# Performance work log

Measured on AMD Instinct MI355X. Metric: run time of the kernel, lower is better.

Reference implementation:

```python
import jax, jax.numpy as jnp
from jax import lax
import numpy as np

T, N, C, S = 256, 64, 7356, 32
NEG = -1e9  # finite stand-in for -inf (keeps grads clean)


def setup_inputs() -> dict:
    key = jax.random.key(0)
    k1, k2, k3 = jax.random.split(key, 3)
    out = jax.random.normal(k1, (T, N, C), dtype=jnp.float32)
    # PyTorch CTCLoss expects log-probs; the module passes `out` through as-is,
    # so we feed log_softmax'd activations (what the surrounding model produces).
    out = jax.nn.log_softmax(out, axis=-1)
    text = jax.random.randint(k2, (N, S), 1, C)            # labels in [1, C-1], blank=0 excluded
    pre_len = jnp.full((N,), T, dtype=jnp.int64 if jax.config.jax_enable_x64 else jnp.int32)
    lengths = jax.random.randint(k3, (N,), 16, S + 1)       # target lengths in [16, 32]
    return {"out": out, "text": text, "pre_len": pre_len, "lengths": lengths}


def _ctc_loss_mean(logp, targets, input_lengths, target_lengths):
    # logp: [T, N, C] log-probs; targets: [N, S]; lengths: [N]
    Tt, Nn, _ = logp.shape
    Ss = targets.shape[1]
    L = 2 * Ss + 1
    # Extended label sequence: blank, l1, blank, l2, ..., blank
    ext = jnp.zeros((Nn, L), dtype=targets.dtype).at[:, 1::2].set(targets)  # [N, L]
    ext_m2 = jnp.concatenate([jnp.zeros((Nn, 2), dtype=ext.dtype), ext[:, :-2]], axis=1)
    skip = (jnp.arange(L)[None, :] >= 2) & (ext != 0) & (ext != ext_m2)      # [N, L]

    # Gather per-frame log-probs of extended labels: [T, N, L]
    lp_ext = logp[:, jnp.arange(Nn)[:, None], ext]

    alpha0 = jnp.full((Nn, L), NEG, dtype=logp.dtype)
    alpha0 = alpha0.at[:, 0].set(lp_ext[0, :, 0]).at[:, 1].set(lp_ext[0, :, 1])

    negcol1 = jnp.full((Nn, 1), NEG, dtype=logp.dtype)
    negcol2 = jnp.full((Nn, 2), NEG, dtype=logp.dtype)

    def step(alpha, lp_t):
        s1 = jnp.concatenate([negcol1, alpha[:, :-1]], axis=1)
        s2 = jnp.concatenate([negcol2, alpha[:, :-2]], axis=1)
        a = jnp.logaddexp(alpha, s1)
        a = jnp.logaddexp(a, jnp.where(skip, s2, NEG))
        new = a + lp_t
        return new, new

    _, alphas_rest = lax.scan(step, alpha0, lp_ext[1:])
    alphas = jnp.concatenate([alpha0[None], alphas_rest], axis=0)  # [T, N, L]

    n_idx = jnp.arange(Nn)
    a_end = alphas[input_lengths - 1, n_idx]                        # [N, L]
    l_last = 2 * target_lengths                                     # index of final blank
    log_like = jnp.logaddexp(a_end[n_idx, l_last], a_end[n_idx, l_last - 1])
    # reduction='mean': per-sample loss / target_length, then mean over batch
    per = -log_like / target_lengths.astype(logp.dtype)
    return jnp.mean(per)


def reference(out, text, pre_len, lengths):
    loss = _ctc_loss_mean(out, text, pre_len, lengths)
    weight = jnp.square(1.0 - jnp.exp(-loss))
    return weight * loss
```

## Files before the change

### kernel.cpp

```cpp
#include <hip/hip_runtime.h>

#define Tt 256
#define Nn 64
#define Cc 7356
#define Ss 32
#define NEGf (-1.0e9f)
#define LOG2E 1.4426950408889634f
#define LN2   0.6931471805599453f
#define PFD 16
#define HT 128

__device__ __forceinline__ float fexp2(float x) { return __builtin_amdgcn_exp2f(x); }
__device__ __forceinline__ float flog2(float x) { return __builtin_amdgcn_logf(x); }

__device__ __forceinline__ float dpp_shr1(float x, float fallback) {
    int r = __builtin_amdgcn_update_dpp(__float_as_int(fallback), __float_as_int(x),
                                        0x138 , 0xf, 0xf, false);
    return __int_as_float(r);
}
__device__ __forceinline__ float dpp_shl1(float x, float fallback) {
    int r = __builtin_amdgcn_update_dpp(__float_as_int(fallback), __float_as_int(x),
                                        0x130 , 0xf, 0xf, false);
    return __int_as_float(r);
}
__device__ __forceinline__ float bcast(float x, int l) {
    return __int_as_float(__builtin_amdgcn_readlane(__float_as_int(x), l));
}
__device__ __forceinline__ float lse2(float a, float b) {
    float m = fmaxf(a, b);
    return m + flog2(fexp2(a - m) + fexp2(b - m));
}

#define COMPACT_FLOATS (Tt * Nn * 64)
#define JV_OFF COMPACT_FLOATS
#define WS_NEED_BYTES ((COMPACT_FLOATS + Nn + 1) * 4)

__global__ __launch_bounds__(256) void ctc_gather_kernel(
    const float* __restrict__ logp, const int* __restrict__ text,
    float* __restrict__ ws)
{
    int gid = blockIdx.x * 256 + threadIdx.x;
    int l  = gid & 63;
    int n  = (gid >> 6) & (Nn - 1);
    int tq = gid >> 12;
    int ch = (l & 1) ? 0 : text[n * Ss + (l >> 1)];
    const float* src = logp + (size_t)n * Cc + ch;
    const size_t tstr = (size_t)Nn * Cc;
    float v0 = src[(size_t)(4 * tq + 0) * tstr];
    float v1 = src[(size_t)(4 * tq + 1) * tstr];
    float v2 = src[(size_t)(4 * tq + 2) * tstr];
    float v3 = src[(size_t)(4 * tq + 3) * tstr];
    float* dst = ws + (size_t)n * 64 + l;
    dst[(size_t)(4 * tq + 0) * (Nn * 64)] = v0 * LOG2E;
    dst[(size_t)(4 * tq + 1) * (Nn * 64)] = v1 * LOG2E;
    dst[(size_t)(4 * tq + 2) * (Nn * 64)] = v2 * LOG2E;
    dst[(size_t)(4 * tq + 3) * (Nn * 64)] = v3 * LOG2E;
    if (gid == 0) {
        int* counter = (int*)(ws + JV_OFF + Nn);
        __hip_atomic_store(counter, 0, __ATOMIC_RELAXED, __HIP_MEMORY_SCOPE_AGENT);
    }
}

__global__ __launch_bounds__(128) void ctc_fbj_kernel(
    const float* __restrict__ compact, const int* __restrict__ text,
    const int* __restrict__ lengths, float* __restrict__ ws,
    float* __restrict__ out)
{
    __shared__ float jpre[65];
    __shared__ float jbeta[65];

    const int lane = threadIdx.x & 63;
    const bool fwd = threadIdx.x < 64;
    const int n    = blockIdx.x;

    int ch = (lane & 1) ? 0 : text[n * Ss + (lane >> 1)];
    int ch_m2 = __shfl_up(ch, 2, 64);
    int ch_p2 = __shfl_down(ch, 2, 64);
    const bool skipd = (lane >= 2) && !(lane & 1) && (ch != ch_m2);
    const bool skips = !(lane & 1) && (lane <= 61) && (ch != ch_p2);

    const float* base = compact + (size_t)n * 64 + lane;
    const int rstride = Nn * 64;
    const int len = lengths[n];

    float stv;
    float st0;

    if (fwd) {
        float lp0 = base[0];
        stv = (lane == 0) ? lp0 : NEGf;
        st0 = bcast(lp0, 1);
        float lpb[PFD];
        #pragma unroll
        for (int i = 0; i < PFD; ++i)
            lpb[i] = base[(size_t)(1 + i) * rstride];
        int t = 1;
        for (int blk = 0; blk < 7; ++blk) {
            #pragma unroll
            for (int j = 0; j < PFD; ++j) {
                float lp = lpb[j];
                int tpf = t + PFD;
                if (tpf <= HT - 1)
                    lpb[j] = base[(size_t)tpf * rstride];
                float lpblank = bcast(lp, 1);
                float s1 = dpp_shr1(stv, st0);
                float s2 = dpp_shr1(s1, NEGf);
                float s2m = skipd ? s2 : NEGf;
                float m  = fmaxf(fmaxf(stv, s1), s2m);
                float e  = fexp2(stv - m) + fexp2(s1 - m) + fexp2(s2m - m);
                stv = (m + lp) + flog2(e);
                st0 = st0 + lpblank;
                ++t;
            }
        }
        #pragma unroll
        for (int j = 0; j < PFD - 1; ++j) {
            float lp = lpb[j];
            float lpblank = bcast(lp, 1);
            float s1 = dpp_shr1(stv, st0);
            float s2 = dpp_shr1(s1, NEGf);
            float s2m = skipd ? s2 : NEGf;
            float m  = fmaxf(fmaxf(stv, s1), s2m);
            float e  = fexp2(stv - m) + fexp2(s1 - m) + fexp2(s2m - m);
            stv = (m + lp) + flog2(e);
            st0 = st0 + lpblank;
        }
        float s1 = dpp_shr1(stv, st0);
        float s2 = dpp_shr1(s1, NEGf);
        float s2m = skipd ? s2 : NEGf;
        float m  = fmaxf(fmaxf(stv, s1), s2m);
        float e  = fexp2(stv - m) + fexp2(s1 - m) + fexp2(s2m - m);
        jpre[1 + lane] = m + flog2(e);
        if (lane == 0) jpre[0] = st0;
    } else {
        float lpT = base[(size_t)(Tt - 1) * rstride];
        int llast = 2 * len;
        stv = (lane == llast - 2 || lane == llast - 1) ? lpT : NEGf;
        st0 = NEGf;
        float lpb[PFD];
        #pragma unroll
        for (int i = 0; i < PFD; ++i)
            lpb[i] = base[(size_t)(Tt - 2 - i) * rstride];
        int t = Tt - 2;
        for (int blk = 0; blk < 7; ++blk) {
            #pragma unroll
            for (int j = 0; j < PFD; ++j) {
                float lp = lpb[j];
                int tpf = t - PFD;
                if (tpf >= HT)
                    lpb[j] = base[(size_t)tpf * rstride];
                float lpblank = bcast(lp, 1);
                float b1 = bcast(stv, 0);
                float u1 = dpp_shl1(stv, NEGf);
                float u2 = dpp_shl1(u1, NEGf);
                float u2m = skips ? u2 : NEGf;
                float m  = fmaxf(fmaxf(stv, u1), u2m);
                float e  = fexp2(stv - m) + fexp2(u1 - m) + fexp2(u2m - m);
                float nb = (m + lp) + flog2(e);
                float m2 = fmaxf(st0, b1);
                st0 = (m2 + lpblank) + flog2(fexp2(st0 - m2) + fexp2(b1 - m2));
                stv = nb;
                --t;
            }
        }
        #pragma unroll
        for (int j = 0; j < PFD - 1; ++j) {
            float lp = lpb[j];
            float lpblank = bcast(lp, 1);
            float b1 = bcast(stv, 0);
            float u1 = dpp_shl1(stv, NEGf);
            float u2 = dpp_shl1(u1, NEGf);
            float u2m = skips ? u2 : NEGf;
            float m  = fmaxf(fmaxf(stv, u1), u2m);
            float e  = fexp2(stv - m) + fexp2(u1 - m) + fexp2(u2m - m);
            float nb = (m + lp) + flog2(e);
            float m2 = fmaxf(st0, b1);
            st0 = (m2 + lpblank) + flog2(fexp2(st0 - m2) + fexp2(b1 - m2));
            stv = nb;
        }
        jbeta[1 + lane] = stv;
        if (lane == 0) jbeta[0] = st0;
    }

    __syncthreads();
    if (!fwd) return;

    float local = jpre[lane] + jbeta[lane];
    if (lane == 0) local = lse2(local, jpre[64] + jbeta[64]);
    #pragma unroll
    for (int off = 1; off < 64; off <<= 1)
        local = lse2(local, __shfl_xor(local, off, 64));
    float per = -(local * LN2) / (float)len;

    float* slots = ws + JV_OFF;
    int* counter = (int*)(ws + JV_OFF + Nn);
    int old = -1;
    if (lane == 0) {
        __hip_atomic_store(&slots[n], per, __ATOMIC_RELEASE, __HIP_MEMORY_SCOPE_AGENT);
        __threadfence();
        old = __hip_atomic_fetch_add(counter, 1, __ATOMIC_ACQ_REL, __HIP_MEMORY_SCOPE_AGENT);
    }
    old = __shfl(old, 0, 64);
    if (old == Nn - 1) {
        __threadfence();
        float v = __hip_atomic_load(&slots[lane], __ATOMIC_ACQUIRE, __HIP_MEMORY_SCOPE_AGENT);
        #pragma unroll
        for (int off = 32; off > 0; off >>= 1)
            v += __shfl_down(v, off, 64);
        if (lane == 0) {
            float loss = v * (1.0f / (float)Nn);
            float w = 1.0f - __expf(-loss);
            out[0] = w * w * loss;
        }
    }
}

__global__ __launch_bounds__(64) void ctc_alpha_kernel(
    const float* __restrict__ logp, const int* __restrict__ text,
    const int* __restrict__ pre_len, const int* __restrict__ lengths,
    float* __restrict__ per_out)
{
    const int n = blockIdx.x; const int lane = threadIdx.x;
    int ch = 0;
    if (lane & 1) ch = text[n * Ss + (lane >> 1)];
    int ch_m2 = __shfl_up(ch, 2, 64);
    bool skip = (lane >= 2) && (ch != 0) && (ch != ch_m2);
    const size_t rowbase = (size_t)n * Cc, tstride = (size_t)Nn * Cc;
    float lp0 = logp[rowbase + ch] * LOG2E;
    float alpha = (lane < 2) ? lp0 : NEGf, alpha64 = NEGf;
    const int stop_t = pre_len[n] - 1;
    float sv = alpha, sv64 = alpha64;
    float lpb[PFD];
    #pragma unroll
    for (int i = 0; i < PFD; ++i)
        lpb[i] = logp[(size_t)(1 + i) * tstride + rowbase + ch] * LOG2E;
#define CTC_STEP(LPREG) { \
        float lp = (LPREG); float lpblank = bcast(lp, 0); float a63 = bcast(alpha, 63); \
        float s1 = dpp_shr1(alpha, NEGf); float s2 = dpp_shr1(s1, NEGf); \
        float s2m = skip ? s2 : NEGf; \
        float m = fmaxf(fmaxf(alpha, s1), s2m); \
        float e = fexp2(alpha - m) + fexp2(s1 - m) + fexp2(s2m - m); \
        float na = (m + lp) + flog2(e); \
        float m2 = fmaxf(alpha64, a63); \
        alpha64 = (m2 + lpblank) + flog2(fexp2(alpha64 - m2) + fexp2(a63 - m2)); \
        alpha = na; if (t == stop_t) { sv = alpha; sv64 = alpha64; } ++t; }
    int t = 1;
    for (int blk = 0; blk < 15; ++blk) {
        #pragma unroll
        for (int j = 0; j < PFD; ++j) {
            float lpj = lpb[j]; int tpf = t + PFD;
            if (tpf < Tt) lpb[j] = logp[(size_t)tpf * tstride + rowbase + ch] * LOG2E;
            CTC_STEP(lpj);
        }
    }
    #pragma unroll
    for (int j = 0; j < PFD - 1; ++j) { CTC_STEP(lpb[j]); }
#undef CTC_STEP
    int len = lengths[n]; int l_last = 2 * len;
    float v1 = __shfl(sv, l_last < 64 ? l_last : 63, 64);
    if (l_last == 64) v1 = sv64;
    float v2 = __shfl(sv, l_last - 1, 64);
    float per = -(lse2(v1, v2) * LN2) / (float)len;
    if (lane == 0) per_out[n] = per;
}

__global__ __launch_bounds__(64) void finalize_kernel(
    const float* __restrict__ per, float* __restrict__ out)
{
    int lane = threadIdx.x;
    float v = per[lane];
    #pragma unroll
    for (int off = 32; off > 0; off >>= 1) v += __shfl_down(v, off, 64);
    if (lane == 0) {
        float loss = v * (1.0f / (float)Nn);
        float w = 1.0f - __expf(-loss);
        out[0] = w * w * loss;
    }
}

extern "C" void kernel_launch(void* const* d_in, const int* in_sizes, int n_in,
                              void* d_out, int out_size, void* d_ws, size_t ws_size,
                              hipStream_t stream) {
    const float* logp    = (const float*)d_in[0];
    const int*   text    = (const int*)d_in[1];
    const int*   pre_len = (const int*)d_in[2];
    const int*   lengths = (const int*)d_in[3];

    if (ws_size >= (size_t)WS_NEED_BYTES) {
        float* ws = (float*)d_ws;
        ctc_gather_kernel<<<(Tt / 4) * Nn * 64 / 256, 256, 0, stream>>>(logp, text, ws);
        ctc_fbj_kernel<<<Nn, 128, 0, stream>>>(ws, text, lengths, ws, (float*)d_out);
    } else {
        float* per = (float*)d_ws;
        ctc_alpha_kernel<<<Nn, 64, 0, stream>>>(logp, text, pre_len, lengths, per);
        finalize_kernel<<<1, 64, 0, stream>>>(per, (float*)d_out);
    }
}
```

Baseline: 30.84 us.

## Split forward and backward CTC passes into separate workgroups joined by atomic counter

The forward and backward recursions, which used to be two wavefronts in one 128-thread block, now run as separate 64-thread blocks, giving 2*N blocks in total. Each pass writes its half-time vector to global workspace, and a per-sample atomic counter picks the second finisher to combine them. The aim is to spread the two serial chains across more compute units and avoid co-scheduling them on one CU. The cost is extra global-memory traffic and fences in place of shared memory, plus a second level of atomics before the final reduction.

Measured after the change: 34.22 us. +11.0%, slower.

```diff
diff --git a/kernel.cpp b/kernel.cpp
--- a/kernel.cpp
+++ b/kernel.cpp
@@ -32,14 +32,17 @@
 }
 
 #define COMPACT_FLOATS (Tt * Nn * 64)
-#define JV_OFF COMPACT_FLOATS
-#define WS_NEED_BYTES ((COMPACT_FLOATS + Nn + 1) * 4)
+#define WS_CTR   COMPACT_FLOATS
+#define WS_SLOTS (WS_CTR + 65)
+#define WS_VEC   (WS_CTR + 129)
+#define WS_NEED_BYTES ((WS_VEC + Nn * 130) * 4)
 
 __global__ __launch_bounds__(256) void ctc_gather_kernel(
     const float* __restrict__ logp, const int* __restrict__ text,
     float* __restrict__ ws)
 {
     int gid = blockIdx.x * 256 + threadIdx.x;
+    if (gid < 65) ((int*)(ws + WS_CTR))[gid] = 0;
     int l  = gid & 63;
     int n  = (gid >> 6) & (Nn - 1);
     int tq = gid >> 12;
@@ -55,23 +58,16 @@
     dst[(size_t)(4 * tq + 1) * (Nn * 64)] = v1 * LOG2E;
     dst[(size_t)(4 * tq + 2) * (Nn * 64)] = v2 * LOG2E;
     dst[(size_t)(4 * tq + 3) * (Nn * 64)] = v3 * LOG2E;
-    if (gid == 0) {
-        int* counter = (int*)(ws + JV_OFF + Nn);
-        __hip_atomic_store(counter, 0, __ATOMIC_RELAXED, __HIP_MEMORY_SCOPE_AGENT);
-    }
-}
-
-__global__ __launch_bounds__(128) void ctc_fbj_kernel(
+}
+
+__global__ __launch_bounds__(64) void ctc_fb_kernel(
     const float* __restrict__ compact, const int* __restrict__ text,
     const int* __restrict__ lengths, float* __restrict__ ws,
     float* __restrict__ out)
 {
-    __shared__ float jpre[65];
-    __shared__ float jbeta[65];
-
-    const int lane = threadIdx.x & 63;
-    const bool fwd = threadIdx.x < 64;
-    const int n    = blockIdx.x;
+    const int lane = threadIdx.x;
+    const int n    = blockIdx.x & (Nn - 1);
+    const bool fwd = blockIdx.x < Nn;
 
     int ch = (lane & 1) ? 0 : text[n * Ss + (lane >> 1)];
     int ch_m2 = __shfl_up(ch, 2, 64);
@@ -82,6 +78,8 @@
     const float* base = compact + (size_t)n * 64 + lane;
     const int rstride = Nn * 64;
     const int len = lengths[n];
+
+    float* vec = ws + WS_VEC + n * 130 + (fwd ? 0 : 65);
 
     float stv;
     float st0;
@@ -130,8 +128,8 @@
         float s2m = skipd ? s2 : NEGf;
         float m  = fmaxf(fmaxf(stv, s1), s2m);
         float e  = fexp2(stv - m) + fexp2(s1 - m) + fexp2(s2m - m);
-        jpre[1 + lane] = m + flog2(e);
-        if (lane == 0) jpre[0] = st0;
+        vec[1 + lane] = m + flog2(e);
+        if (lane == 0) vec[0] = st0;
     } else {
         float lpT = base[(size_t)(Tt - 1) * rstride];
         int llast = 2 * len;
@@ -178,23 +176,35 @@
             st0 = (m2 + lpblank) + flog2(fexp2(st0 - m2) + fexp2(b1 - m2));
             stv = nb;
         }
-        jbeta[1 + lane] = stv;
-        if (lane == 0) jbeta[0] = st0;
-    }
-
-    __syncthreads();
-    if (!fwd) return;
-
-    float local = jpre[lane] + jbeta[lane];
-    if (lane == 0) local = lse2(local, jpre[64] + jbeta[64]);
+        vec[1 + lane] = stv;
+        if (lane == 0) vec[0] = st0;
+    }
+
+    __threadfence();
+    int* pair = (int*)(ws + WS_CTR) + 1;
+    int old = -1;
+    if (lane == 0)
+        old = __hip_atomic_fetch_add(&pair[n], 1, __ATOMIC_ACQ_REL, __HIP_MEMORY_SCOPE_AGENT);
+    old = __shfl(old, 0, 64);
+    if (old == 0) return;
+
+    const float* va = ws + WS_VEC + n * 130;
+    const float* vb = va + 65;
+    float local = __hip_atomic_load(&va[lane], __ATOMIC_ACQUIRE, __HIP_MEMORY_SCOPE_AGENT)
+                + __hip_atomic_load(&vb[lane], __ATOMIC_ACQUIRE, __HIP_MEMORY_SCOPE_AGENT);
+    if (lane == 0) {
+        float a64 = __hip_atomic_load(&va[64], __ATOMIC_ACQUIRE, __HIP_MEMORY_SCOPE_AGENT)
+                  + __hip_atomic_load(&vb[64], __ATOMIC_ACQUIRE, __HIP_MEMORY_SCOPE_AGENT);
+        local = lse2(local, a64);
+    }
     #pragma unroll
     for (int off = 1; off < 64; off <<= 1)
         local = lse2(local, __shfl_xor(local, off, 64));
     float per = -(local * LN2) / (float)len;
 
-    float* slots = ws + JV_OFF;
-    int* counter = (int*)(ws + JV_OFF + Nn);
-    int old = -1;
+    float* slots = ws + WS_SLOTS;
+    int* counter = (int*)(ws + WS_CTR);
+    old = -1;
     if (lane == 0) {
         __hip_atomic_store(&slots[n], per, __ATOMIC_RELEASE, __HIP_MEMORY_SCOPE_AGENT);
         __threadfence();
@@ -288,8 +298,8 @@
 
     if (ws_size >= (size_t)WS_NEED_BYTES) {
         float* ws = (float*)d_ws;
-        ctc_gather_kernel<<<(Tt / 4) * Nn * 64 / 256, 256, 0, stream>>>(logp, text, ws);
-        ctc_fbj_kernel<<<Nn, 128, 0, stream>>>(ws, text, lengths, ws, (float*)d_out);
+        ctc_gather_kernel<<<COMPACT_FLOATS / 4 / 256, 256, 0, stream>>>(logp, text, ws);
+        ctc_fb_kernel<<<2 * Nn, 64, 0, stream>>>(ws, text, lengths, ws, (float*)d_out);
     } else {
         float* per = (float*)d_ws;
         ctc_alpha_kernel<<<Nn, 64, 0, stream>>>(logp, text, pre_len, lengths, per);
```
